# Performance work log

Measured on AMD Instinct MI355X. Metric: run time of the kernel, lower is better.

Reference implementation:

```python
import jax, jax.numpy as jnp
import numpy as np

NODE_DIM, HID, NCLS = 16, 64, 2
B, T, N = 16, 64, 400


def setup_inputs() -> dict:
    key = jax.random.key(0)
    ks = jax.random.split(key, 10)
    s = lambda k, shape: jax.random.normal(k, shape, dtype=jnp.float32) * 0.05
    return {
        "x_seq": jax.random.normal(ks[0], (B, T, N, NODE_DIM), dtype=jnp.float32),
        "adj_seq": jax.random.uniform(ks[1], (B, T, N, N), dtype=jnp.float32),
        "Wp": s(ks[2], (NODE_DIM, HID)),
        "bp": s(ks[3], (HID,)),
        "W_ih": s(ks[4], (3 * HID, HID)),
        "W_hh": s(ks[5], (3 * HID, HID)),
        "b_ih": s(ks[6], (3 * HID,)),
        "b_hh": s(ks[7], (3 * HID,)),
        "Wc": s(ks[8], (HID, NCLS)),
        "bc": s(ks[9], (NCLS,)),
    }


def _gru_last(feats, W_ih, W_hh, b_ih, b_hh):
    # feats: [B, T, H] -> final hidden state [B, H] (torch nn.GRU equations)
    H = W_hh.shape[1]

    def step(h, x_t):
        gi = x_t @ W_ih.T + b_ih            # [B, 3H]
        gh = h @ W_hh.T + b_hh              # [B, 3H]
        i_r, i_z, i_n = gi[:, :H], gi[:, H:2 * H], gi[:, 2 * H:]
        h_r, h_z, h_n = gh[:, :H], gh[:, H:2 * H], gh[:, 2 * H:]
        r = jax.nn.sigmoid(i_r + h_r)
        z = jax.nn.sigmoid(i_z + h_z)
        n = jnp.tanh(i_n + r * h_n)
        h_new = (1.0 - z) * n + z * h
        return h_new, None

    h0 = jnp.zeros((feats.shape[0], H), dtype=feats.dtype)
    h_last, _ = jax.lax.scan(step, h0, jnp.swapaxes(feats, 0, 1))  # scan over T
    return h_last


def reference(x_seq, adj_seq, Wp, bp, W_ih, W_hh, b_ih, b_hh, Wc, bc):
    n_nodes = x_seq.shape[2]
    # node projection for all (b, t) at once: [B, T, N, H]
    h = jnp.einsum('btnd,dh->btnh', x_seq, Wp) + bp
    # adjacency aggregation + mean pool over nodes, fused: mean_n (adj @ h)
    feats = jnp.einsum('btnm,btmh->bth', adj_seq, h) / n_nodes  # [B, T, H]
    z = _gru_last(feats, W_ih, W_hh, b_ih, b_hh)                 # [B, H]
    logits = z @ Wc + bc                                         # [B, NCLS]
    return logits
```

## Files before the change

kernel.cpp:

```cpp
#include <hip/hip_runtime.h>

#define NDIM 16
#define HID  64
#define G3   192
#define NCLS 2
#define BB   16
#define TT   64
#define NN   400

__global__ __launch_bounds__(512) void feats_gi_kernel(
    const float* __restrict__ x_seq,
    const float* __restrict__ adj_seq,
    const float* __restrict__ Wp,
    const float* __restrict__ bp,
    const float* __restrict__ W_ih,
    const float* __restrict__ b_ih,
    float* __restrict__ gi_out)
{
    const int bt = blockIdx.x;
    const float* __restrict__ adj = adj_seq + (size_t)bt * NN * NN;
    const float* __restrict__ xbt = x_seq   + (size_t)bt * NN * NDIM;
    const int tid = threadIdx.x;

    __shared__ float4 cpart[4][100];
    __shared__ float  colsum[NN];
    __shared__ float  wred[8][17];
    __shared__ float  yf[17];
    __shared__ float  ffin[HID];

    const int mq = tid & 127;
    const int nr = tid >> 7;
    if (mq < 100) {
        float4 cs = make_float4(0.f, 0.f, 0.f, 0.f);
        const float* base = adj + mq * 4 + (size_t)nr * NN;
        #pragma unroll 8
        for (int i = 0; i < 100; i++) {
            float4 v = *reinterpret_cast<const float4*>(base + (size_t)i * 4 * NN);
            cs.x += v.x; cs.y += v.y; cs.z += v.z; cs.w += v.w;
        }
        cpart[nr][mq] = cs;
    }
    __syncthreads();
    if (tid < 100) {
        float4 a = cpart[0][tid], b = cpart[1][tid];
        float4 c = cpart[2][tid], d = cpart[3][tid];
        colsum[tid * 4 + 0] = (a.x + b.x) + (c.x + d.x);
        colsum[tid * 4 + 1] = (a.y + b.y) + (c.y + d.y);
        colsum[tid * 4 + 2] = (a.z + b.z) + (c.z + d.z);
        colsum[tid * 4 + 3] = (a.w + b.w) + (c.w + d.w);
    }
    __syncthreads();

    float y[17];
    #pragma unroll
    for (int i = 0; i < 17; i++) y[i] = 0.f;
    if (tid < NN) {
        const int m = tid;
        float c = colsum[m];
        y[16] = c;
        const float4* xp = reinterpret_cast<const float4*>(xbt + m * NDIM);
        float4 v0 = xp[0], v1 = xp[1], v2 = xp[2], v3 = xp[3];
        y[0]  = c * v0.x;  y[1]  = c * v0.y;  y[2]  = c * v0.z;  y[3]  = c * v0.w;
        y[4]  = c * v1.x;  y[5]  = c * v1.y;  y[6]  = c * v1.z;  y[7]  = c * v1.w;
        y[8]  = c * v2.x;  y[9]  = c * v2.y;  y[10] = c * v2.z;  y[11] = c * v2.w;
        y[12] = c * v3.x;  y[13] = c * v3.y;  y[14] = c * v3.z;  y[15] = c * v3.w;
    }
    #pragma unroll
    for (int off = 32; off >= 1; off >>= 1) {
        #pragma unroll
        for (int i = 0; i < 17; i++) y[i] += __shfl_down(y[i], off, 64);
    }
    const int lane = tid & 63;
    const int wv   = tid >> 6;
    if (lane == 0) {
        #pragma unroll
        for (int i = 0; i < 17; i++) wred[wv][i] = y[i];
    }
    __syncthreads();
    if (tid < 17) {
        float s = 0.f;
        #pragma unroll
        for (int w = 0; w < 8; w++) s += wred[w][tid];
        yf[tid] = s;
    }
    __syncthreads();

    if (tid < HID) {
        float acc = 0.f;
        #pragma unroll
        for (int d = 0; d < NDIM; d++) acc += yf[d] * Wp[d * HID + tid];
        ffin[tid] = (acc + yf[16] * bp[tid]) * (1.0f / (float)NN);
    }
    __syncthreads();

    if (tid < G3) {
        const float4* wr = reinterpret_cast<const float4*>(W_ih + tid * HID);
        float acc = b_ih[tid];
        #pragma unroll
        for (int k4 = 0; k4 < HID / 4; k4++) {
            float4 w = wr[k4];
            acc += ffin[4 * k4 + 0] * w.x + ffin[4 * k4 + 1] * w.y
                 + ffin[4 * k4 + 2] * w.z + ffin[4 * k4 + 3] * w.w;
        }
        gi_out[(size_t)bt * G3 + tid] = acc;
    }
}

__global__ __launch_bounds__(192) void gru_kernel(
    const float* __restrict__ gi_all,
    const float* __restrict__ W_hh,
    const float* __restrict__ b_hh,
    const float* __restrict__ Wc,
    const float* __restrict__ bc,
    float* __restrict__ out)
{
    const int b = blockIdx.x;
    const int j = threadIdx.x;

    float whh[HID];
    #pragma unroll
    for (int k4 = 0; k4 < HID / 4; k4++) {
        float4 w = *reinterpret_cast<const float4*>(W_hh + j * HID + 4 * k4);
        whh[4 * k4 + 0] = w.x; whh[4 * k4 + 1] = w.y;
        whh[4 * k4 + 2] = w.z; whh[4 * k4 + 3] = w.w;
    }
    const float bh = b_hh[j];

    __shared__ __align__(16) float hst[HID];
    __shared__ float rbuf[HID], zbuf[HID], inb[HID], hnb[HID];
    float hreg = 0.f;
    if (j < HID) hst[j] = 0.f;
    __syncthreads();

    const float* __restrict__ gi = gi_all + (size_t)b * TT * G3;
    float gcur = gi[j];

    for (int t = 0; t < TT; t++) {
        float gnext = (t + 1 < TT) ? gi[(t + 1) * G3 + j] : 0.f;

        float gh = bh;
        #pragma unroll
        for (int k4 = 0; k4 < HID / 4; k4++) {
            float4 h4 = *reinterpret_cast<const float4*>(hst + 4 * k4);
            gh += h4.x * whh[4 * k4 + 0] + h4.y * whh[4 * k4 + 1]
                + h4.z * whh[4 * k4 + 2] + h4.w * whh[4 * k4 + 3];
        }

        float g = gcur + gh;
        if (j < 64) {
            rbuf[j] = 1.f / (1.f + expf(-g));
        } else if (j < 128) {
            zbuf[j - 64] = 1.f / (1.f + expf(-g));
        } else {
            inb[j - 128] = gcur;
            hnb[j - 128] = gh;
        }
        __syncthreads();

        if (j < HID) {
            float nv = tanhf(inb[j] + rbuf[j] * hnb[j]);
            float z  = zbuf[j];
            hreg = (1.f - z) * nv + z * hreg;
            hst[j] = hreg;
        }
        __syncthreads();
        gcur = gnext;
    }

    if (j < NCLS) {
        float acc = bc[j];
        #pragma unroll
        for (int h = 0; h < HID; h++) acc += hst[h] * Wc[h * NCLS + j];
        out[b * NCLS + j] = acc;
    }
}

extern "C" void kernel_launch(void* const* d_in, const int* in_sizes, int n_in,
                              void* d_out, int out_size, void* d_ws, size_t ws_size,
                              hipStream_t stream) {
    const float* x_seq   = (const float*)d_in[0];
    const float* adj_seq = (const float*)d_in[1];
    const float* Wp      = (const float*)d_in[2];
    const float* bp      = (const float*)d_in[3];
    const float* W_ih    = (const float*)d_in[4];
    const float* W_hh    = (const float*)d_in[5];
    const float* b_ih    = (const float*)d_in[6];
    const float* b_hh    = (const float*)d_in[7];
    const float* Wc      = (const float*)d_in[8];
    const float* bc      = (const float*)d_in[9];

    float* gi  = (float*)d_ws;
    float* out = (float*)d_out;

    feats_gi_kernel<<<BB * TT, 512, 0, stream>>>(x_seq, adj_seq, Wp, bp,
                                                 W_ih, b_ih, gi);
    gru_kernel<<<BB, 192, 0, stream>>>(gi, W_hh, b_hh, Wc, bc, out);
}
```

Baseline: 174.6 us.

## Split adjacency column-sum into separate kernel and restructure GRU to one wave

```diff
diff --git a/kernel.cpp b/kernel.cpp
--- a/kernel.cpp
+++ b/kernel.cpp
@@ -7,10 +7,36 @@
 #define BB   16
 #define TT   64
 #define NN   400
-
-__global__ __launch_bounds__(512) void feats_gi_kernel(
+#define NQ   4
+#define QROWS (NN / NQ)
+
+#define GI_OFS (8u << 20)
+
+__global__ __launch_bounds__(128) void colsum_kernel(
+    const float* __restrict__ adj_seq,
+    float4* __restrict__ part4)
+{
+    const int g  = blockIdx.x;
+    const int bt = g >> 2;
+    const int q  = g & 3;
+    const int t  = threadIdx.x;
+    if (t >= 100) return;
+
+    const float* __restrict__ base =
+        adj_seq + (size_t)bt * NN * NN + (size_t)q * QROWS * NN + t * 4;
+
+    float4 cs = make_float4(0.f, 0.f, 0.f, 0.f);
+    #pragma unroll 10
+    for (int i = 0; i < QROWS; i++) {
+        float4 v = *reinterpret_cast<const float4*>(base + (size_t)i * NN);
+        cs.x += v.x; cs.y += v.y; cs.z += v.z; cs.w += v.w;
+    }
+    part4[(size_t)g * 100 + t] = cs;
+}
+
+__global__ __launch_bounds__(256) void tile_kernel(
     const float* __restrict__ x_seq,
-    const float* __restrict__ adj_seq,
+    const float4* __restrict__ part4,
     const float* __restrict__ Wp,
     const float* __restrict__ bp,
     const float* __restrict__ W_ih,
@@ -18,52 +44,42 @@
     float* __restrict__ gi_out)
 {
     const int bt = blockIdx.x;
-    const float* __restrict__ adj = adj_seq + (size_t)bt * NN * NN;
-    const float* __restrict__ xbt = x_seq   + (size_t)bt * NN * NDIM;
     const int tid = threadIdx.x;
-
-    __shared__ float4 cpart[4][100];
-    __shared__ float  colsum[NN];
-    __shared__ float  wred[8][17];
-    __shared__ float  yf[17];
-    __shared__ float  ffin[HID];
-
-    const int mq = tid & 127;
-    const int nr = tid >> 7;
-    if (mq < 100) {
-        float4 cs = make_float4(0.f, 0.f, 0.f, 0.f);
-        const float* base = adj + mq * 4 + (size_t)nr * NN;
-        #pragma unroll 8
-        for (int i = 0; i < 100; i++) {
-            float4 v = *reinterpret_cast<const float4*>(base + (size_t)i * 4 * NN);
-            cs.x += v.x; cs.y += v.y; cs.z += v.z; cs.w += v.w;
-        }
-        cpart[nr][mq] = cs;
-    }
-    __syncthreads();
+    const float* __restrict__ xbt = x_seq + (size_t)bt * NN * NDIM;
+
+    __shared__ __align__(16) float colsum[NN];
+    __shared__ float wred[4][17];
+    __shared__ float yf[17];
+    __shared__ float ffin[HID];
+
     if (tid < 100) {
-        float4 a = cpart[0][tid], b = cpart[1][tid];
-        float4 c = cpart[2][tid], d = cpart[3][tid];
-        colsum[tid * 4 + 0] = (a.x + b.x) + (c.x + d.x);
-        colsum[tid * 4 + 1] = (a.y + b.y) + (c.y + d.y);
-        colsum[tid * 4 + 2] = (a.z + b.z) + (c.z + d.z);
-        colsum[tid * 4 + 3] = (a.w + b.w) + (c.w + d.w);
+        const float4* p = part4 + (size_t)bt * NQ * 100 + tid;
+        float4 a = p[0], b = p[100], c = p[200], d = p[300];
+        float4 s;
+        s.x = (a.x + b.x) + (c.x + d.x);
+        s.y = (a.y + b.y) + (c.y + d.y);
+        s.z = (a.z + b.z) + (c.z + d.z);
+        s.w = (a.w + b.w) + (c.w + d.w);
+        reinterpret_cast<float4*>(colsum)[tid] = s;
     }
     __syncthreads();
 
     float y[17];
     #pragma unroll
     for (int i = 0; i < 17; i++) y[i] = 0.f;
-    if (tid < NN) {
-        const int m = tid;
-        float c = colsum[m];
-        y[16] = c;
-        const float4* xp = reinterpret_cast<const float4*>(xbt + m * NDIM);
-        float4 v0 = xp[0], v1 = xp[1], v2 = xp[2], v3 = xp[3];
-        y[0]  = c * v0.x;  y[1]  = c * v0.y;  y[2]  = c * v0.z;  y[3]  = c * v0.w;
-        y[4]  = c * v1.x;  y[5]  = c * v1.y;  y[6]  = c * v1.z;  y[7]  = c * v1.w;
-        y[8]  = c * v2.x;  y[9]  = c * v2.y;  y[10] = c * v2.z;  y[11] = c * v2.w;
-        y[12] = c * v3.x;  y[13] = c * v3.y;  y[14] = c * v3.z;  y[15] = c * v3.w;
+    #pragma unroll
+    for (int r = 0; r < 2; r++) {
+        const int m = tid + r * 256;
+        if (m < NN) {
+            float c = colsum[m];
+            y[16] += c;
+            const float4* xp = reinterpret_cast<const float4*>(xbt + m * NDIM);
+            float4 v0 = xp[0], v1 = xp[1], v2 = xp[2], v3 = xp[3];
+            y[0]  += c * v0.x;  y[1]  += c * v0.y;  y[2]  += c * v0.z;  y[3]  += c * v0.w;
+            y[4]  += c * v1.x;  y[5]  += c * v1.y;  y[6]  += c * v1.z;  y[7]  += c * v1.w;
+            y[8]  += c * v2.x;  y[9]  += c * v2.y;  y[10] += c * v2.z;  y[11] += c * v2.w;
+            y[12] += c * v3.x;  y[13] += c * v3.y;  y[14] += c * v3.z;  y[15] += c * v3.w;
+        }
     }
     #pragma unroll
     for (int off = 32; off >= 1; off >>= 1) {
@@ -78,10 +94,7 @@
     }
     __syncthreads();
     if (tid < 17) {
-        float s = 0.f;
-        #pragma unroll
-        for (int w = 0; w < 8; w++) s += wred[w][tid];
-        yf[tid] = s;
+        yf[tid] = (wred[0][tid] + wred[1][tid]) + (wred[2][tid] + wred[3][tid]);
     }
     __syncthreads();
 
@@ -106,7 +119,7 @@
     }
 }
 
-__global__ __launch_bounds__(192) void gru_kernel(
+__global__ __launch_bounds__(64, 1) void gru_kernel(
     const float* __restrict__ gi_all,
     const float* __restrict__ W_hh,
     const float* __restrict__ b_hh,
@@ -117,61 +130,69 @@
     const int b = blockIdx.x;
     const int j = threadIdx.x;
 
-    float whh[HID];
+    float wr_[HID], wz_[HID], wn_[HID];
     #pragma unroll
     for (int k4 = 0; k4 < HID / 4; k4++) {
-        float4 w = *reinterpret_cast<const float4*>(W_hh + j * HID + 4 * k4);
-        whh[4 * k4 + 0] = w.x; whh[4 * k4 + 1] = w.y;
-        whh[4 * k4 + 2] = w.z; whh[4 * k4 + 3] = w.w;
-    }
-    const float bh = b_hh[j];
-
-    __shared__ __align__(16) float hst[HID];
-    __shared__ float rbuf[HID], zbuf[HID], inb[HID], hnb[HID];
-    float hreg = 0.f;
-    if (j < HID) hst[j] = 0.f;
-    __syncthreads();
+        float4 a = *reinterpret_cast<const float4*>(W_hh + (j)       * HID + 4 * k4);
+        float4 c = *reinterpret_cast<const float4*>(W_hh + (j + 64)  * HID + 4 * k4);
+        float4 d = *reinterpret_cast<const float4*>(W_hh + (j + 128) * HID + 4 * k4);
+        wr_[4*k4+0]=a.x; wr_[4*k4+1]=a.y; wr_[4*k4+2]=a.z; wr_[4*k4+3]=a.w;
+        wz_[4*k4+0]=c.x; wz_[4*k4+1]=c.y; wz_[4*k4+2]=c.z; wz_[4*k4+3]=c.w;
+        wn_[4*k4+0]=d.x; wn_[4*k4+1]=d.y; wn_[4*k4+2]=d.z; wn_[4*k4+3]=d.w;
+    }
+    const float bhr = b_hh[j], bhz = b_hh[j + 64], bhn = b_hh[j + 128];
+
+    __shared__ __align__(16) float hls[HID];
+    float h = 0.f;
 
     const float* __restrict__ gi = gi_all + (size_t)b * TT * G3;
-    float gcur = gi[j];
+    float gr = gi[j], gz = gi[j + 64], gn = gi[j + 128];
 
     for (int t = 0; t < TT; t++) {
-        float gnext = (t + 1 < TT) ? gi[(t + 1) * G3 + j] : 0.f;
-
-        float gh = bh;
+        hls[j] = h;
+        __syncthreads();
+
+        float gr2 = 0.f, gz2 = 0.f, gn2 = 0.f;
+        if (t + 1 < TT) {
+            const float* gnx = gi + (t + 1) * G3;
+            gr2 = gnx[j]; gz2 = gnx[j + 64]; gn2 = gnx[j + 128];
+        }
+
+        float ar0 = bhr, ar1 = 0.f, az0 = bhz, az1 = 0.f, an0 = bhn, an1 = 0.f;
         #pragma unroll
         for (int k4 = 0; k4 < HID / 4; k4++) {
-            float4 h4 = *reinterpret_cast<const float4*>(hst + 4 * k4);
-            gh += h4.x * whh[4 * k4 + 0] + h4.y * whh[4 * k4 + 1]
-                + h4.z * whh[4 * k4 + 2] + h4.w * whh[4 * k4 + 3];
-        }
-
-        float g = gcur + gh;
-        if (j < 64) {
-            rbuf[j] = 1.f / (1.f + expf(-g));
-        } else if (j < 128) {
-            zbuf[j - 64] = 1.f / (1.f + expf(-g));
-        } else {
-            inb[j - 128] = gcur;
-            hnb[j - 128] = gh;
-        }
+            float4 hv = reinterpret_cast<const float4*>(hls)[k4];
+            if (k4 & 1) {
+                ar1 += hv.x*wr_[4*k4+0] + hv.y*wr_[4*k4+1] + hv.z*wr_[4*k4+2] + hv.w*wr_[4*k4+3];
+                az1 += hv.x*wz_[4*k4+0] + hv.y*wz_[4*k4+1] + hv.z*wz_[4*k4+2] + hv.w*wz_[4*k4+3];
+                an1 += hv.x*wn_[4*k4+0] + hv.y*wn_[4*k4+1] + hv.z*wn_[4*k4+2] + hv.w*wn_[4*k4+3];
+            } else {
+                ar0 += hv.x*wr_[4*k4+0] + hv.y*wr_[4*k4+1] + hv.z*wr_[4*k4+2] + hv.w*wr_[4*k4+3];
+                az0 += hv.x*wz_[4*k4+0] + hv.y*wz_[4*k4+1] + hv.z*wz_[4*k4+2] + hv.w*wz_[4*k4+3];
+                an0 += hv.x*wn_[4*k4+0] + hv.y*wn_[4*k4+1] + hv.z*wn_[4*k4+2] + hv.w*wn_[4*k4+3];
+            }
+        }
+        float ghr = ar0 + ar1, ghz = az0 + az1, ghn = an0 + an1;
+
+        float r  = 1.f / (1.f + expf(-(gr + ghr)));
+        float z  = 1.f / (1.f + expf(-(gz + ghz)));
+        float nv = tanhf(gn + r * ghn);
+        h = (1.f - z) * nv + z * h;
         __syncthreads();
 
-        if (j < HID) {
-            float nv = tanhf(inb[j] + rbuf[j] * hnb[j]);
-            float z  = zbuf[j];
-            hreg = (1.f - z) * nv + z * hreg;
-            hst[j] = hreg;
-        }
-        __syncthreads();
-        gcur = gnext;
-    }
-
-    if (j < NCLS) {
-        float acc = bc[j];
-        #pragma unroll
-        for (int h = 0; h < HID; h++) acc += hst[h] * Wc[h * NCLS + j];
-        out[b * NCLS + j] = acc;
+        gr = gr2; gz = gz2; gn = gn2;
+    }
+
+    float c0 = h * Wc[j * NCLS + 0];
+    float c1 = h * Wc[j * NCLS + 1];
+    #pragma unroll
+    for (int off = 32; off >= 1; off >>= 1) {
+        c0 += __shfl_down(c0, off, 64);
+        c1 += __shfl_down(c1, off, 64);
+    }
+    if (j == 0) {
+        out[b * NCLS + 0] = c0 + bc[0];
+        out[b * NCLS + 1] = c1 + bc[1];
     }
 }
 
@@ -189,10 +210,11 @@
     const float* Wc      = (const float*)d_in[8];
     const float* bc      = (const float*)d_in[9];
 
-    float* gi  = (float*)d_ws;
-    float* out = (float*)d_out;
-
-    feats_gi_kernel<<<BB * TT, 512, 0, stream>>>(x_seq, adj_seq, Wp, bp,
-                                                 W_ih, b_ih, gi);
-    gru_kernel<<<BB, 192, 0, stream>>>(gi, W_hh, b_hh, Wc, bc, out);
-}
+    float4* part4 = (float4*)d_ws;
+    float*  gi    = (float*)((char*)d_ws + GI_OFS);
+    float*  outp  = (float*)d_out;
+
+    colsum_kernel<<<BB * TT * NQ, 128, 0, stream>>>(adj_seq, part4);
+    tile_kernel<<<BB * TT, 256, 0, stream>>>(x_seq, part4, Wp, bp, W_ih, b_ih, gi);
+    gru_kernel<<<BB, 64, 0, stream>>>(gi, W_hh, b_hh, Wc, bc, outp);
+}
```

Result: slower. 206.8 us (+18.4%).

## Flatten adjacency column-sum loads with nontemporal loads and speed up GRU math

Applied to the files above, without the earlier changes.

```diff
diff --git a/kernel.cpp b/kernel.cpp
--- a/kernel.cpp
+++ b/kernel.cpp
@@ -8,7 +8,9 @@
 #define TT   64
 #define NN   400
 
-__global__ __launch_bounds__(512) void feats_gi_kernel(
+typedef float v4f __attribute__((ext_vector_type(4)));
+
+__global__ __launch_bounds__(512, 6) void feats_gi_kernel(
     const float* __restrict__ x_seq,
     const float* __restrict__ adj_seq,
     const float* __restrict__ Wp,
@@ -17,37 +19,32 @@
     const float* __restrict__ b_ih,
     float* __restrict__ gi_out)
 {
-    const int bt = blockIdx.x;
-    const float* __restrict__ adj = adj_seq + (size_t)bt * NN * NN;
-    const float* __restrict__ xbt = x_seq   + (size_t)bt * NN * NDIM;
+    const int bt  = blockIdx.x;
     const int tid = threadIdx.x;
-
-    __shared__ float4 cpart[4][100];
-    __shared__ float  colsum[NN];
-    __shared__ float  wred[8][17];
-    __shared__ float  yf[17];
-    __shared__ float  ffin[HID];
-
-    const int mq = tid & 127;
-    const int nr = tid >> 7;
-    if (mq < 100) {
-        float4 cs = make_float4(0.f, 0.f, 0.f, 0.f);
-        const float* base = adj + mq * 4 + (size_t)nr * NN;
-        #pragma unroll 8
-        for (int i = 0; i < 100; i++) {
-            float4 v = *reinterpret_cast<const float4*>(base + (size_t)i * 4 * NN);
-            cs.x += v.x; cs.y += v.y; cs.z += v.z; cs.w += v.w;
-        }
-        cpart[nr][mq] = cs;
+    const float* __restrict__ xbt = x_seq + (size_t)bt * NN * NDIM;
+
+    __shared__ v4f   cpart[5][100];
+    __shared__ __align__(16) float colsum[NN];
+    __shared__ float wred[8][17];
+    __shared__ float yf[17];
+    __shared__ float ffin[HID];
+
+    if (tid < 500) {
+        const v4f* __restrict__ base =
+            reinterpret_cast<const v4f*>(adj_seq + (size_t)bt * NN * NN) + tid;
+        v4f cs = (v4f)(0.f);
+        #pragma unroll 10
+        for (int k = 0; k < 80; k++) {
+            v4f v = __builtin_nontemporal_load(base + 500 * k);
+            cs += v;
+        }
+        cpart[tid / 100][tid % 100] = cs;
     }
     __syncthreads();
     if (tid < 100) {
-        float4 a = cpart[0][tid], b = cpart[1][tid];
-        float4 c = cpart[2][tid], d = cpart[3][tid];
-        colsum[tid * 4 + 0] = (a.x + b.x) + (c.x + d.x);
-        colsum[tid * 4 + 1] = (a.y + b.y) + (c.y + d.y);
-        colsum[tid * 4 + 2] = (a.z + b.z) + (c.z + d.z);
-        colsum[tid * 4 + 3] = (a.w + b.w) + (c.w + d.w);
+        v4f s = ((cpart[0][tid] + cpart[1][tid]) +
+                 (cpart[2][tid] + cpart[3][tid])) + cpart[4][tid];
+        *reinterpret_cast<v4f*>(colsum + 4 * tid) = s;
     }
     __syncthreads();
 
@@ -106,6 +103,16 @@
     }
 }
 
+__device__ __forceinline__ float fast_sigmoid(float x) {
+    x = fminf(fmaxf(x, -20.f), 20.f);
+    return __builtin_amdgcn_rcpf(1.f + __expf(-x));
+}
+__device__ __forceinline__ float fast_tanh(float x) {
+    x = fminf(fmaxf(x, -10.f), 10.f);
+    float e2 = __expf(2.f * x);
+    return (e2 - 1.f) * __builtin_amdgcn_rcpf(e2 + 1.f);
+}
+
 __global__ __launch_bounds__(192) void gru_kernel(
     const float* __restrict__ gi_all,
     const float* __restrict__ W_hh,
@@ -138,19 +145,24 @@
     for (int t = 0; t < TT; t++) {
         float gnext = (t + 1 < TT) ? gi[(t + 1) * G3 + j] : 0.f;
 
-        float gh = bh;
-        #pragma unroll
-        for (int k4 = 0; k4 < HID / 4; k4++) {
-            float4 h4 = *reinterpret_cast<const float4*>(hst + 4 * k4);
-            gh += h4.x * whh[4 * k4 + 0] + h4.y * whh[4 * k4 + 1]
-                + h4.z * whh[4 * k4 + 2] + h4.w * whh[4 * k4 + 3];
-        }
-
-        float g = gcur + gh;
+        float a0 = 0.f, a1 = 0.f, a2 = 0.f, a3 = 0.f;
+        #pragma unroll
+        for (int k4 = 0; k4 < HID / 4; k4 += 4) {
+            float4 h0 = *reinterpret_cast<const float4*>(hst + 4 * (k4 + 0));
+            float4 h1 = *reinterpret_cast<const float4*>(hst + 4 * (k4 + 1));
+            float4 h2 = *reinterpret_cast<const float4*>(hst + 4 * (k4 + 2));
+            float4 h3 = *reinterpret_cast<const float4*>(hst + 4 * (k4 + 3));
+            a0 += h0.x*whh[4*k4+0]  + h0.y*whh[4*k4+1]  + h0.z*whh[4*k4+2]  + h0.w*whh[4*k4+3];
+            a1 += h1.x*whh[4*k4+4]  + h1.y*whh[4*k4+5]  + h1.z*whh[4*k4+6]  + h1.w*whh[4*k4+7];
+            a2 += h2.x*whh[4*k4+8]  + h2.y*whh[4*k4+9]  + h2.z*whh[4*k4+10] + h2.w*whh[4*k4+11];
+            a3 += h3.x*whh[4*k4+12] + h3.y*whh[4*k4+13] + h3.z*whh[4*k4+14] + h3.w*whh[4*k4+15];
+        }
+        float gh = ((a0 + a1) + (a2 + a3)) + bh;
+
         if (j < 64) {
-            rbuf[j] = 1.f / (1.f + expf(-g));
+            rbuf[j] = fast_sigmoid(gcur + gh);
         } else if (j < 128) {
-            zbuf[j - 64] = 1.f / (1.f + expf(-g));
+            zbuf[j - 64] = fast_sigmoid(gcur + gh);
         } else {
             inb[j - 128] = gcur;
             hnb[j - 128] = gh;
@@ -158,7 +170,7 @@
         __syncthreads();
 
         if (j < HID) {
-            float nv = tanhf(inb[j] + rbuf[j] * hnb[j]);
+            float nv = fast_tanh(inb[j] + rbuf[j] * hnb[j]);
             float z  = zbuf[j];
             hreg = (1.f - z) * nv + z * hreg;
             hst[j] = hreg;
```

Result: faster. 148.1 us (median of 2 runs) (-15.2%).
